# Kernel optimization log

Hardware: AMD Instinct MI355X
Metric: run time of the kernel (lower is better)

The kernel has to match this reference:

```python
import jax, jax.numpy as jnp
import numpy as np

N = 10000
IN_F = 512
OUT_F = 64
ALPHA = 0.2
NEG_INF = -9e15


def setup_inputs() -> dict:
    key = jax.random.key(0)
    k1, k2, k3, k4, k5, k6 = jax.random.split(key, 6)
    x = jax.random.normal(k1, (N, IN_F), dtype=jnp.float32)
    adj = jax.random.randint(k2, (N, N), 0, 2).astype(jnp.float32)
    M = jax.random.uniform(k3, (N, N), dtype=jnp.float32)
    W = jax.random.normal(k4, (IN_F, OUT_F), dtype=jnp.float32) * (1.414 / np.sqrt(IN_F))
    a_self = jax.random.normal(k5, (OUT_F, 1), dtype=jnp.float32) * 0.1
    a_neighs = jax.random.normal(k6, (OUT_F, 1), dtype=jnp.float32) * 0.1
    return {"x": x, "adj": adj, "M": M, "W": W, "a_self": a_self, "a_neighs": a_neighs}


def reference(x, adj, M, W, a_self, a_neighs):
    # h: [N, out_features]
    h = x @ W
    attn_for_self = h @ a_self      # [N, 1]
    attn_for_neighs = h @ a_neighs  # [N, 1]
    # outer-sum broadcast -> [N, N]
    attn_dense = attn_for_self + attn_for_neighs.T
    attn_dense = attn_dense * M
    attn_dense = jax.nn.leaky_relu(attn_dense, negative_slope=ALPHA)
    scores = jnp.where(adj > 0, attn_dense, NEG_INF)
    attention = jax.nn.softmax(scores, axis=1)
    h_prime = attention @ h  # [N, out_features]
    return jax.nn.elu(h_prime)  # concat=True path
```

## Files before the change

### kernel.cpp

```cpp
#include <hip/hip_runtime.h>
#include <math.h>

#define Nn 10000
#define NPAD 10048
#define INF_ 512
#define OUTF 64
#define ALPHA 0.2f
#define LOG2E 1.4426950408889634f

#define TI 32
#define TJ 64
#define NTILES ((Nn + TJ - 1) / TJ)
#define YS 4
#define TPC ((NTILES + YS - 1) / YS)

typedef __attribute__((ext_vector_type(8))) short bfrag;
typedef __attribute__((ext_vector_type(4))) float facc;

#define WS_S    0
#define WS_T    (Nn)
#define WS_TMAX (2*Nn)
#define WS_DEN  (2*Nn + 16)
#define WS_HBT  (3*Nn + 16)

__device__ __forceinline__ unsigned short f2bf(float f) {
    unsigned int u = __float_as_uint(f);
    u += 0x7fffu + ((u >> 16) & 1u);
    return (unsigned short)(u >> 16);
}
__device__ __forceinline__ unsigned int pk2(float a, float b) {
    return (unsigned int)f2bf(a) | ((unsigned int)f2bf(b) << 16);
}

__global__ __launch_bounds__(256) void hgemm_kernel(
    const float* __restrict__ x, const float* __restrict__ W,
    const float* __restrict__ a_self, const float* __restrict__ a_neighs,
    unsigned short* __restrict__ hbfT, float* __restrict__ s, float* __restrict__ t)
{
    const int col  = threadIdx.x & 63;
    const int wid  = threadIdx.x >> 6;
    const int row0 = blockIdx.x * 16 + wid * 4;
    const float* x0 = x + row0 * INF_;

    float acc0 = 0.f, acc1 = 0.f, acc2 = 0.f, acc3 = 0.f;
    #pragma unroll 4
    for (int k4 = 0; k4 < INF_ / 4; ++k4) {
        const int k = k4 << 2;
        const float w0 = W[(k    ) * OUTF + col];
        const float w1 = W[(k + 1) * OUTF + col];
        const float w2 = W[(k + 2) * OUTF + col];
        const float w3 = W[(k + 3) * OUTF + col];
        const float4 xa = *(const float4*)(x0 +          k);
        const float4 xb = *(const float4*)(x0 +   INF_ + k);
        const float4 xc = *(const float4*)(x0 + 2*INF_ + k);
        const float4 xd = *(const float4*)(x0 + 3*INF_ + k);
        acc0 = fmaf(xa.x,w0, fmaf(xa.y,w1, fmaf(xa.z,w2, fmaf(xa.w,w3, acc0))));
        acc1 = fmaf(xb.x,w0, fmaf(xb.y,w1, fmaf(xb.z,w2, fmaf(xb.w,w3, acc1))));
        acc2 = fmaf(xc.x,w0, fmaf(xc.y,w1, fmaf(xc.z,w2, fmaf(xc.w,w3, acc2))));
        acc3 = fmaf(xd.x,w0, fmaf(xd.y,w1, fmaf(xd.z,w2, fmaf(xd.w,w3, acc3))));
    }
    ushort4 hb;
    hb.x = f2bf(acc0); hb.y = f2bf(acc1); hb.z = f2bf(acc2); hb.w = f2bf(acc3);
    *(ushort4*)(hbfT + (size_t)col * NPAD + row0) = hb;

    const float as = a_self[col], an = a_neighs[col];
    #define RED(ACC, U) { \
        float vs = (ACC) * as, vn = (ACC) * an; \
        _Pragma("unroll") \
        for (int d_ = 32; d_; d_ >>= 1) { vs += __shfl_xor(vs, d_); vn += __shfl_xor(vn, d_); } \
        if (col == 0) { s[row0 + (U)] = vs; t[row0 + (U)] = vn; } }
    RED(acc0, 0) RED(acc1, 1) RED(acc2, 2) RED(acc3, 3)
    #undef RED
}

__global__ __launch_bounds__(1024) void tmax_kernel(
    const float* __restrict__ t, float* __restrict__ tmax)
{
    __shared__ float red[16];
    float m = -3e38f;
    for (int i = threadIdx.x; i < Nn; i += 1024) m = fmaxf(m, t[i]);
    #pragma unroll
    for (int d = 32; d; d >>= 1) m = fmaxf(m, __shfl_xor(m, d));
    if ((threadIdx.x & 63) == 0) red[threadIdx.x >> 6] = m;
    __syncthreads();
    if (threadIdx.x < 16) {
        m = red[threadIdx.x];
        #pragma unroll
        for (int d = 8; d; d >>= 1) m = fmaxf(m, __shfl_xor(m, d));
        if (threadIdx.x == 0) *tmax = m;
    }
}

__global__ __launch_bounds__(256, 4) void gat_main_kernel(
    const float* __restrict__ adj, const float* __restrict__ Mm,
    const unsigned short* __restrict__ hbfT, const float* __restrict__ sv,
    const float* __restrict__ tv, const float* __restrict__ tmaxp,
    float* __restrict__ den_acc, float* __restrict__ hp_acc)
{
    __shared__ __align__(16) unsigned short hTl[OUTF][TJ + 8];
    __shared__ __align__(16) unsigned short Pl[TI][TJ + 8];

    const int tid = threadIdx.x;
    const int i0  = blockIdx.x * TI;
    const int tlo = blockIdx.y * TPC;
    const int thi = min(NTILES, tlo + TPC);

    const int rr = tid >> 3, jc = tid & 7;
    const int prow = i0 + rr;
    const bool rowok = prow < Nn;
    const float si = rowok ? sv[prow] : 0.0f;
    const float mc = fmaxf(0.0f, si + *tmaxp) * LOG2E;
    const float* aRow = adj + (size_t)prow * Nn;
    const float* mRow = Mm  + (size_t)prow * Nn;

    const int hc_ = tid >> 2, hseg = tid & 3;
    const unsigned short* hsrc = hbfT + (size_t)hc_ * NPAD + hseg * 16;

    const int lane = tid & 63, wv = tid >> 6;
    const int rb = wv & 1, cbp = wv >> 1;
    const unsigned short* aP  = &Pl[rb * 16 + (lane & 15)][(lane >> 4) * 8];
    const unsigned short* bP0 = &hTl[cbp * 32 + (lane & 15)][(lane >> 4) * 8];
    const unsigned short* bP1 = bP0 + 16 * (TJ + 8);

    facc accA = {0.f, 0.f, 0.f, 0.f}, accB = {0.f, 0.f, 0.f, 0.f};
    float denacc = 0.0f;

    const float4 z4 = make_float4(0.f, 0.f, 0.f, 0.f);
    float4 pa0 = z4, pa1 = z4, pm0 = z4, pm1 = z4, pt0 = z4, pt1 = z4;
    uint4 ph0 = make_uint4(0,0,0,0), ph1 = make_uint4(0,0,0,0);

    auto prefetch = [&](int tile) {
        const int j0 = tile * TJ;
        ph0 = *(const uint4*)(hsrc + j0);
        ph1 = *(const uint4*)(hsrc + j0 + 8);
        const int jl = j0 + (jc << 3);
        if (rowok && jl + 7 < Nn) {
            pa0 = *(const float4*)(aRow + jl); pa1 = *(const float4*)(aRow + jl + 4);
            pm0 = *(const float4*)(mRow + jl); pm1 = *(const float4*)(mRow + jl + 4);
            pt0 = *(const float4*)(tv   + jl); pt1 = *(const float4*)(tv   + jl + 4);
        } else {
            pa0 = pa1 = pm0 = pm1 = pt0 = pt1 = z4;
            if (rowok) {
                #define LD1(dst, base, off) if ((jl + (off)) < Nn) dst = (base)[jl + (off)]
                LD1(pa0.x, aRow, 0); LD1(pa0.y, aRow, 1); LD1(pa0.z, aRow, 2); LD1(pa0.w, aRow, 3);
                LD1(pa1.x, aRow, 4); LD1(pa1.y, aRow, 5); LD1(pa1.z, aRow, 6); LD1(pa1.w, aRow, 7);
                LD1(pm0.x, mRow, 0); LD1(pm0.y, mRow, 1); LD1(pm0.z, mRow, 2); LD1(pm0.w, mRow, 3);
                LD1(pm1.x, mRow, 4); LD1(pm1.y, mRow, 5); LD1(pm1.z, mRow, 6); LD1(pm1.w, mRow, 7);
                LD1(pt0.x, tv,   0); LD1(pt0.y, tv,   1); LD1(pt0.z, tv,   2); LD1(pt0.w, tv,   3);
                LD1(pt1.x, tv,   4); LD1(pt1.y, tv,   5); LD1(pt1.z, tv,   6); LD1(pt1.w, tv,   7);
                #undef LD1
            }
        }
    };

    #define PC(dst, av, mv, tvv) { \
        float e_ = (si + (tvv)) * (mv); \
        float l_ = fmaxf(e_, ALPHA * e_); \
        dst = ((av) > 0.0f) ? exp2f(fmaf(l_, LOG2E, -mc)) : 0.0f; }

    prefetch(tlo);
    for (int tile = tlo; tile < thi; ++tile) {
        __syncthreads();

        *(uint4*)&hTl[hc_][hseg * 16]     = ph0;
        *(uint4*)&hTl[hc_][hseg * 16 + 8] = ph1;

        float4 p40, p41;
        PC(p40.x, pa0.x, pm0.x, pt0.x); PC(p40.y, pa0.y, pm0.y, pt0.y);
        PC(p40.z, pa0.z, pm0.z, pt0.z); PC(p40.w, pa0.w, pm0.w, pt0.w);
        PC(p41.x, pa1.x, pm1.x, pt1.x); PC(p41.y, pa1.y, pm1.y, pt1.y);
        PC(p41.z, pa1.z, pm1.z, pt1.z); PC(p41.w, pa1.w, pm1.w, pt1.w);
        denacc += ((p40.x + p40.y) + (p40.z + p40.w)) + ((p41.x + p41.y) + (p41.z + p41.w));

        uint4 pw;
        pw.x = pk2(p40.x, p40.y); pw.y = pk2(p40.z, p40.w);
        pw.z = pk2(p41.x, p41.y); pw.w = pk2(p41.z, p41.w);
        *(uint4*)&Pl[rr][jc << 3] = pw;

        __syncthreads();

        if (tile + 1 < thi) prefetch(tile + 1);

        #pragma unroll
        for (int k0 = 0; k0 < TJ; k0 += 32) {
            const bfrag af = *(const bfrag*)(aP  + k0);
            const bfrag b0 = *(const bfrag*)(bP0 + k0);
            const bfrag b1 = *(const bfrag*)(bP1 + k0);
            accA = __builtin_amdgcn_mfma_f32_16x16x32_bf16(af, b0, accA, 0, 0, 0);
            accB = __builtin_amdgcn_mfma_f32_16x16x32_bf16(af, b1, accB, 0, 0, 0);
        }
    }
    #undef PC

    float d = denacc;
    d += __shfl_xor(d, 1); d += __shfl_xor(d, 2); d += __shfl_xor(d, 4);
    if (rowok && jc == 0) atomicAdd(&den_acc[prow], d);

    const int orow = i0 + rb * 16 + ((lane >> 4) << 2);
    const int oc   = cbp * 32 + (lane & 15);
    #pragma unroll
    for (int r = 0; r < 4; ++r) {
        if (orow + r < Nn) {
            atomicAdd(&hp_acc[(orow + r) * OUTF + oc],      accA[r]);
            atomicAdd(&hp_acc[(orow + r) * OUTF + oc + 16], accB[r]);
        }
    }
}

__global__ __launch_bounds__(256) void finalize_kernel(
    const float* __restrict__ den, float* __restrict__ out)
{
    const int idx = blockIdx.x * 256 + threadIdx.x;
    const float v = out[idx] / den[idx >> 6];
    out[idx] = (v > 0.0f) ? v : expm1f(v);
}

extern "C" void kernel_launch(void* const* d_in, const int* in_sizes, int n_in,
                              void* d_out, int out_size, void* d_ws, size_t ws_size,
                              hipStream_t stream) {
    const float* x        = (const float*)d_in[0];
    const float* adj      = (const float*)d_in[1];
    const float* Mm       = (const float*)d_in[2];
    const float* W        = (const float*)d_in[3];
    const float* a_self   = (const float*)d_in[4];
    const float* a_neighs = (const float*)d_in[5];

    float* out  = (float*)d_out;
    float* ws   = (float*)d_ws;
    float* s    = ws + WS_S;
    float* t    = ws + WS_T;
    float* tmax = ws + WS_TMAX;
    float* den  = ws + WS_DEN;
    unsigned short* hbfT = (unsigned short*)(ws + WS_HBT);

    hipMemsetAsync(den, 0, Nn * sizeof(float), stream);
    hipMemsetAsync(hbfT, 0, (size_t)OUTF * NPAD * sizeof(unsigned short), stream);
    hipMemsetAsync(d_out, 0, (size_t)out_size * sizeof(float), stream);

    hgemm_kernel<<<Nn / 16, 256, 0, stream>>>(x, W, a_self, a_neighs, hbfT, s, t);
    tmax_kernel<<<1, 1024, 0, stream>>>(t, tmax);
    gat_main_kernel<<<dim3((Nn + TI - 1) / TI, YS), 256, 0, stream>>>(
        adj, Mm, hbfT, s, t, tmax, den, out);
    finalize_kernel<<<(Nn * OUTF) / 256, 256, 0, stream>>>(den, out);
}
```

Baseline: 254.3 us.

## Double-buffer LDS tiles and replace atomic accumulation with per-split partial buffers

The main kernel now keeps two LDS buffers for the P and h tiles. It computes and stages the next tile after issuing the MFMAs on the current one, so each tile needs one barrier instead of two and global loads can run further ahead. Each y-split block writes its numerator and denominator partials to its own slice of workspace instead of using atomicAdd. The finalize kernel sums the four slices, which also removes the three memsets. The cost is twice the LDS (which may lower occupancy) and extra workspace traffic for the partials. The zeroing of the padded hbfT region is dropped, which may matter if the padding is never written.

```diff
diff --git a/kernel.cpp b/kernel.cpp
--- a/kernel.cpp
+++ b/kernel.cpp
@@ -21,7 +21,8 @@
 #define WS_T    (Nn)
 #define WS_TMAX (2*Nn)
 #define WS_DEN  (2*Nn + 16)
-#define WS_HBT  (3*Nn + 16)
+#define WS_HP   (WS_DEN + YS*Nn)
+#define WS_HBT  (WS_HP + YS*Nn*OUTF)
 
 __device__ __forceinline__ unsigned short f2bf(float f) {
     unsigned int u = __float_as_uint(f);
@@ -95,10 +96,10 @@
     const float* __restrict__ adj, const float* __restrict__ Mm,
     const unsigned short* __restrict__ hbfT, const float* __restrict__ sv,
     const float* __restrict__ tv, const float* __restrict__ tmaxp,
-    float* __restrict__ den_acc, float* __restrict__ hp_acc)
-{
-    __shared__ __align__(16) unsigned short hTl[OUTF][TJ + 8];
-    __shared__ __align__(16) unsigned short Pl[TI][TJ + 8];
+    float* __restrict__ den_part, float* __restrict__ hp_part)
+{
+    __shared__ __align__(16) unsigned short hTl[2][OUTF][TJ + 8];
+    __shared__ __align__(16) unsigned short Pl[2][TI][TJ + 8];
 
     const int tid = threadIdx.x;
     const int i0  = blockIdx.x * TI;
@@ -117,10 +118,8 @@
     const unsigned short* hsrc = hbfT + (size_t)hc_ * NPAD + hseg * 16;
 
     const int lane = tid & 63, wv = tid >> 6;
+    const int l15 = lane & 15, kq = lane >> 4;
     const int rb = wv & 1, cbp = wv >> 1;
-    const unsigned short* aP  = &Pl[rb * 16 + (lane & 15)][(lane >> 4) * 8];
-    const unsigned short* bP0 = &hTl[cbp * 32 + (lane & 15)][(lane >> 4) * 8];
-    const unsigned short* bP1 = bP0 + 16 * (TJ + 8);
 
     facc accA = {0.f, 0.f, 0.f, 0.f}, accB = {0.f, 0.f, 0.f, 0.f};
     float denacc = 0.0f;
@@ -158,29 +157,32 @@
         float l_ = fmaxf(e_, ALPHA * e_); \
         dst = ((av) > 0.0f) ? exp2f(fmaf(l_, LOG2E, -mc)) : 0.0f; }
 
-    prefetch(tlo);
-    for (int tile = tlo; tile < thi; ++tile) {
-        __syncthreads();
-
-        *(uint4*)&hTl[hc_][hseg * 16]     = ph0;
-        *(uint4*)&hTl[hc_][hseg * 16 + 8] = ph1;
-
+    auto stage = [&](int b) {
+        *(uint4*)&hTl[b][hc_][hseg * 16]     = ph0;
+        *(uint4*)&hTl[b][hc_][hseg * 16 + 8] = ph1;
         float4 p40, p41;
         PC(p40.x, pa0.x, pm0.x, pt0.x); PC(p40.y, pa0.y, pm0.y, pt0.y);
         PC(p40.z, pa0.z, pm0.z, pt0.z); PC(p40.w, pa0.w, pm0.w, pt0.w);
         PC(p41.x, pa1.x, pm1.x, pt1.x); PC(p41.y, pa1.y, pm1.y, pt1.y);
         PC(p41.z, pa1.z, pm1.z, pt1.z); PC(p41.w, pa1.w, pm1.w, pt1.w);
         denacc += ((p40.x + p40.y) + (p40.z + p40.w)) + ((p41.x + p41.y) + (p41.z + p41.w));
-
         uint4 pw;
         pw.x = pk2(p40.x, p40.y); pw.y = pk2(p40.z, p40.w);
         pw.z = pk2(p41.x, p41.y); pw.w = pk2(p41.z, p41.w);
-        *(uint4*)&Pl[rr][jc << 3] = pw;
-
+        *(uint4*)&Pl[b][rr][jc << 3] = pw;
+    };
+
+    prefetch(tlo);
+    stage(0);
+    if (tlo + 1 < thi) prefetch(tlo + 1);
+
+    for (int tile = tlo; tile < thi; ++tile) {
+        const int cur = (tile - tlo) & 1;
         __syncthreads();
 
-        if (tile + 1 < thi) prefetch(tile + 1);
-
+        const unsigned short* aP  = &Pl[cur][rb * 16 + l15][kq * 8];
+        const unsigned short* bP0 = &hTl[cur][cbp * 32 + l15][kq * 8];
+        const unsigned short* bP1 = bP0 + 16 * (TJ + 8);
         #pragma unroll
         for (int k0 = 0; k0 < TJ; k0 += 32) {
             const bfrag af = *(const bfrag*)(aP  + k0);
@@ -189,29 +191,40 @@
             accA = __builtin_amdgcn_mfma_f32_16x16x32_bf16(af, b0, accA, 0, 0, 0);
             accB = __builtin_amdgcn_mfma_f32_16x16x32_bf16(af, b1, accB, 0, 0, 0);
         }
+
+        if (tile + 1 < thi) {
+            stage(cur ^ 1);
+            if (tile + 2 < thi) prefetch(tile + 2);
+        }
     }
     #undef PC
 
     float d = denacc;
     d += __shfl_xor(d, 1); d += __shfl_xor(d, 2); d += __shfl_xor(d, 4);
-    if (rowok && jc == 0) atomicAdd(&den_acc[prow], d);
-
-    const int orow = i0 + rb * 16 + ((lane >> 4) << 2);
-    const int oc   = cbp * 32 + (lane & 15);
+    if (rowok && jc == 0) den_part[blockIdx.y * Nn + prow] = d;
+
+    float* hp = hp_part + (size_t)blockIdx.y * (Nn * OUTF);
+    const int orow = i0 + rb * 16 + (kq << 2);
+    const int oc   = cbp * 32 + l15;
     #pragma unroll
     for (int r = 0; r < 4; ++r) {
         if (orow + r < Nn) {
-            atomicAdd(&hp_acc[(orow + r) * OUTF + oc],      accA[r]);
-            atomicAdd(&hp_acc[(orow + r) * OUTF + oc + 16], accB[r]);
+            hp[(orow + r) * OUTF + oc]      = accA[r];
+            hp[(orow + r) * OUTF + oc + 16] = accB[r];
         }
     }
 }
 
 __global__ __launch_bounds__(256) void finalize_kernel(
-    const float* __restrict__ den, float* __restrict__ out)
+    const float* __restrict__ dp, const float* __restrict__ hp,
+    float* __restrict__ out)
 {
     const int idx = blockIdx.x * 256 + threadIdx.x;
-    const float v = out[idx] / den[idx >> 6];
+    const int S = Nn * OUTF;
+    const float num = (hp[idx] + hp[S + idx]) + (hp[2*S + idx] + hp[3*S + idx]);
+    const int row = idx >> 6;
+    const float den = (dp[row] + dp[Nn + row]) + (dp[2*Nn + row] + dp[3*Nn + row]);
+    const float v = num / den;
     out[idx] = (v > 0.0f) ? v : expm1f(v);
 }
 
@@ -230,16 +243,13 @@
     float* s    = ws + WS_S;
     float* t    = ws + WS_T;
     float* tmax = ws + WS_TMAX;
-    float* den  = ws + WS_DEN;
+    float* denp = ws + WS_DEN;
+    float* hpp  = ws + WS_HP;
     unsigned short* hbfT = (unsigned short*)(ws + WS_HBT);
-
-    hipMemsetAsync(den, 0, Nn * sizeof(float), stream);
-    hipMemsetAsync(hbfT, 0, (size_t)OUTF * NPAD * sizeof(unsigned short), stream);
-    hipMemsetAsync(d_out, 0, (size_t)out_size * sizeof(float), stream);
 
     hgemm_kernel<<<Nn / 16, 256, 0, stream>>>(x, W, a_self, a_neighs, hbfT, s, t);
     tmax_kernel<<<1, 1024, 0, stream>>>(t, tmax);
     gat_main_kernel<<<dim3((Nn + TI - 1) / TI, YS), 256, 0, stream>>>(
-        adj, Mm, hbfT, s, t, tmax, den, out);
-    finalize_kernel<<<(Nn * OUTF) / 256, 256, 0, stream>>>(den, out);
-}
+        adj, Mm, hbfT, s, t, tmax, denp, hpp);
+    finalize_kernel<<<(Nn * OUTF) / 256, 256, 0, stream>>>(denp, hpp, out);
+}
```

Result: slower. 261.4 us (+2.8%).
